# Optimization experiments

Measured on AMD Instinct MI355X. Metric: run time of the kernel, lower is better.

## Reference

```python
import jax, jax.numpy as jnp
import numpy as np

B, C, N, F = 256, 4, 64, 256   # batch, in_channels, neighbors, in_features
OC, OF = 8, 256                # out_channels, out_features


def setup_inputs() -> dict:
    key = jax.random.key(0)
    k1, k2, k3, k4, k5 = jax.random.split(key, 5)
    x = jax.random.normal(k1, (B, C, F), dtype=jnp.float32)
    neighbor = jax.random.normal(k2, (B, N, C, F), dtype=jnp.float32)
    # torch.nn.Linear weights are (out_features, in_features)
    W_att1 = jax.random.normal(k3, (C, F), dtype=jnp.float32) / np.sqrt(F).astype(np.float32)
    W_att2 = jax.random.normal(k4, (C, F), dtype=jnp.float32) / np.sqrt(F).astype(np.float32)
    # Conv1d weight: (out_c*out_f, 2C, F); kernel_size==F makes it a dense contraction
    W_conv = jax.random.normal(k5, (OC * OF, 2 * C, F), dtype=jnp.float32) / np.sqrt(2 * C * F).astype(np.float32)
    return {"x": x, "neighbor": neighbor, "W_att1": W_att1, "W_att2": W_att2, "W_conv": W_conv}


def reference(x, neighbor, W_att1, W_att2, W_conv):
    # --- attention weights: einsum 'ci,nkl->n' = sum(att1(x_i)) * sum_{k,l} att2(y_i)[n]
    s1 = jnp.sum(x @ W_att1.T, axis=(1, 2))              # (B,)
    s2 = jnp.sum(neighbor @ W_att2.T, axis=(2, 3))       # (B, N)
    w = jax.nn.softmax(s1[:, None] * s2, axis=1)         # softmax over neighbors (dim 0 per-sample)

    # --- feature adjacency: einsum 'ca,ncb,n->cab' vectorized over batch
    fadj = jnp.einsum('bcx,bncy,bn->bcxy', x, neighbor, w)   # (B, C, F, F)
    fadj = fadj + jnp.swapaxes(fadj, -1, -2)
    # sgnroot
    fadj = jnp.sign(fadj) * jnp.sqrt(jnp.clip(jnp.abs(fadj), 1e-8, None))
    # row normalize over dim -2, NaN -> 0
    adj = fadj / (jnp.abs(fadj).sum(axis=-2, keepdims=True) + 1e-7)
    adj = jnp.where(jnp.isnan(adj), jnp.float32(0.0), adj)

    # --- transform: cat([adj @ x, x], channel) then full-width conv1d (dense contraction)
    h = jnp.einsum('bcxy,bcy->bcx', adj, x)              # (B, C, F)
    z = jnp.concatenate([h, x], axis=1)                  # (B, 2C, F)
    out = jnp.einsum('bcf,ocf->bo', z, W_conv).reshape(B, OC, OF)
    return out, adj
```

## Files before the change

kernel.cpp:

```cpp
#include <hip/hip_runtime.h>
#include <hip/hip_bf16.h>
#include <math.h>


typedef __bf16 bf16x8 __attribute__((ext_vector_type(8)));
typedef __bf16 bf16x4 __attribute__((ext_vector_type(4)));
typedef float f32x4 __attribute__((ext_vector_type(4)));

#define NB 256
#define NC 4
#define NN 64
#define NF 256
#define NO 2048

__global__ __launch_bounds__(256) void k_pre(
    const float* __restrict__ x, const float* __restrict__ nb,
    const float* __restrict__ W1, const float* __restrict__ W2,
    float* __restrict__ s1, float* __restrict__ s2)
{
  __shared__ float w2s[256], w1s[256];
  int t = threadIdx.x;
  int w = t >> 6, l = t & 63;

  w2s[t] = W2[t] + W2[256 + t] + W2[512 + t] + W2[768 + t];
  w1s[t] = W1[t] + W1[256 + t] + W1[512 + t] + W1[768 + t];
  __syncthreads();

  int gw = blockIdx.x * 4 + w;
  float4 wv2 = *(const float4*)&w2s[l * 4];
  float4 wv1 = *(const float4*)&w1s[l * 4];
  for (int task = gw; task < 16640; task += 8192) {
    bool isS2 = task < 16384;
    const float4* src = isS2 ? ((const float4*)nb + (size_t)task * 256)
                             : ((const float4*)x + (size_t)(task - 16384) * 256);
    float4 wv = isS2 ? wv2 : wv1;
    float val = 0.f;
    #pragma unroll
    for (int k = 0; k < 4; ++k) {
      float4 v = src[l + 64 * k];
      val += v.x * wv.x + v.y * wv.y + v.z * wv.z + v.w * wv.w;
    }
    for (int off = 32; off > 0; off >>= 1) val += __shfl_down(val, off);
    if (l == 0) {
      if (isS2) s2[task] = val;
      else s1[task - 16384] = val;
    }
  }
}

__global__ __launch_bounds__(256) void k_adj(
    const float* __restrict__ x, const float* __restrict__ nb,
    const float* __restrict__ Wc,
    const float* __restrict__ s1, const float* __restrict__ s2,
    float* __restrict__ adj, __hip_bfloat16* __restrict__ zbf,
    __hip_bfloat16* __restrict__ Wcb)
{
  __shared__ float xs[256], ns[256], invs[256], wsh[64];
  __shared__ float part[4][256];
  int t = threadIdx.x;
  int w = t >> 6, l = t & 63;
  int blk = blockIdx.x;
  int b = blk >> 2, c = blk & 3;

  {
    const float4* Wc4 = (const float4*)Wc;
    bf16x4* Wcb4 = (bf16x4*)Wcb;
    #pragma unroll
    for (int q = 0; q < 4; ++q) {
      int idx = blk * 1024 + q * 256 + t;
      float4 v = Wc4[idx];
      bf16x4 o = { (__bf16)v.x, (__bf16)v.y, (__bf16)v.z, (__bf16)v.w };
      Wcb4[idx] = o;
    }
  }

  if (t < 64) {
    float v = s1[b] * s2[b * 64 + t];
    float m = v;
    for (int off = 32; off > 0; off >>= 1) m = fmaxf(m, __shfl_xor(m, off));
    float e = expf(v - m);
    float s = e;
    for (int off = 32; off > 0; off >>= 1) s += __shfl_xor(s, off);
    wsh[t] = e / s;
  }
  float xval = x[(size_t)blk * 256 + t];
  xs[t] = xval;
  zbf[(size_t)b * 2048 + 1024 + c * 256 + t] = __float2bfloat16(xval);
  __syncthreads();

  const float4* nb4 = (const float4*)(nb + (size_t)b * 65536 + c * 256);
  float4 a4 = {0.f, 0.f, 0.f, 0.f};
  #pragma unroll
  for (int k = 0; k < 16; ++k) {
    int n = w + 4 * k;
    float4 v = nb4[(size_t)n * 256 + l];
    float wn = wsh[n];
    a4.x = fmaf(wn, v.x, a4.x);
    a4.y = fmaf(wn, v.y, a4.y);
    a4.z = fmaf(wn, v.z, a4.z);
    a4.w = fmaf(wn, v.w, a4.w);
  }
  *(float4*)&part[w][l * 4] = a4;
  __syncthreads();
  ns[t] = part[0][t] + part[1][t] + part[2][t] + part[3][t];
  __syncthreads();

  int j0 = l * 4;
  float4 xv = *(const float4*)&xs[j0];
  float4 nv = *(const float4*)&ns[j0];
  int i0 = w * 64;

  float4 cs = {0.f, 0.f, 0.f, 0.f};
  #pragma unroll 4
  for (int ii = 0; ii < 64; ++ii) {
    int i = i0 + ii;
    float xi = xs[i], ni = ns[i];
    cs.x += __builtin_amdgcn_sqrtf(fmaxf(fabsf(fmaf(xi, nv.x, xv.x * ni)), 1e-8f));
    cs.y += __builtin_amdgcn_sqrtf(fmaxf(fabsf(fmaf(xi, nv.y, xv.y * ni)), 1e-8f));
    cs.z += __builtin_amdgcn_sqrtf(fmaxf(fabsf(fmaf(xi, nv.z, xv.z * ni)), 1e-8f));
    cs.w += __builtin_amdgcn_sqrtf(fmaxf(fabsf(fmaf(xi, nv.w, xv.w * ni)), 1e-8f));
  }
  *(float4*)&part[w][j0] = cs;
  __syncthreads();
  invs[t] = 1.f / (part[0][t] + part[1][t] + part[2][t] + part[3][t] + 1e-7f);
  __syncthreads();

  float4 iv = *(const float4*)&invs[j0];
  float4 ha = {0.f, 0.f, 0.f, 0.f};
  float* ab = adj + (size_t)blk * 65536;
  #pragma unroll 4
  for (int ii = 0; ii < 64; ++ii) {
    int i = i0 + ii;
    float xi = xs[i], ni = ns[i];
    float pix = invs[i] * xi;
    float v0 = fmaf(xi, nv.x, xv.x * ni);
    float v1 = fmaf(xi, nv.y, xv.y * ni);
    float v2 = fmaf(xi, nv.z, xv.z * ni);
    float v3 = fmaf(xi, nv.w, xv.w * ni);
    float g0 = copysignf(__builtin_amdgcn_sqrtf(fmaxf(fabsf(v0), 1e-8f)), v0);
    float g1 = copysignf(__builtin_amdgcn_sqrtf(fmaxf(fabsf(v1), 1e-8f)), v1);
    float g2 = copysignf(__builtin_amdgcn_sqrtf(fmaxf(fabsf(v2), 1e-8f)), v2);
    float g3 = copysignf(__builtin_amdgcn_sqrtf(fmaxf(fabsf(v3), 1e-8f)), v3);
    f32x4 o = { g0 * iv.x, g1 * iv.y, g2 * iv.z, g3 * iv.w };
    __builtin_nontemporal_store(o, (f32x4*)&ab[(size_t)i * 256 + j0]);
    ha.x = fmaf(g0, pix, ha.x);
    ha.y = fmaf(g1, pix, ha.y);
    ha.z = fmaf(g2, pix, ha.z);
    ha.w = fmaf(g3, pix, ha.w);
  }
  __syncthreads();
  *(float4*)&part[w][j0] = ha;
  __syncthreads();
  float hsum = part[0][t] + part[1][t] + part[2][t] + part[3][t];
  zbf[(size_t)b * 2048 + c * 256 + t] = __float2bfloat16(hsum);
}

__global__ __launch_bounds__(256) void k_gemm(
    const __hip_bfloat16* __restrict__ zb, const __hip_bfloat16* __restrict__ Wcb,
    float* __restrict__ out)
{
  __shared__ __hip_bfloat16 Al[2][64][136];
  __shared__ __hip_bfloat16 Bl[2][64][136];
  int t = threadIdx.x;
  int wave = t >> 6, lane = t & 63;
  int g = lane >> 4, r = lane & 15;
  int mh = wave >> 1, nh = wave & 1;
  int bm = blockIdx.x & 3, bn = blockIdx.x >> 2;

  f32x4 acc00 = {0.f,0.f,0.f,0.f}, acc01 = {0.f,0.f,0.f,0.f};
  f32x4 acc10 = {0.f,0.f,0.f,0.f}, acc11 = {0.f,0.f,0.f,0.f};

  const float4* zb4 = (const float4*)zb;
  const float4* wc4 = (const float4*)Wcb;

  #pragma unroll
  for (int q = 0; q < 4; ++q) {
    int idx = q * 256 + t;
    int row = idx >> 4, c16 = idx & 15;
    float4 va = zb4[(size_t)(bm * 64 + row) * 256 + c16];
    *(float4*)&Al[0][row][c16 * 8] = va;
    float4 vb = wc4[(size_t)(bn * 64 + row) * 256 + c16];
    *(float4*)&Bl[0][row][c16 * 8] = vb;
  }
  __syncthreads();

  int cur = 0;
  for (int kb = 0; kb < 16; ++kb) {
    float4 va[4], vb[4];
    if (kb < 15) {
      #pragma unroll
      for (int q = 0; q < 4; ++q) {
        int idx = q * 256 + t;
        int row = idx >> 4, c16 = idx & 15;
        va[q] = zb4[(size_t)(bm * 64 + row) * 256 + (kb + 1) * 16 + c16];
        vb[q] = wc4[(size_t)(bn * 64 + row) * 256 + (kb + 1) * 16 + c16];
      }
    }
    #pragma unroll
    for (int kk = 0; kk < 4; ++kk) {
      bf16x8 a0 = *(const bf16x8*)&Al[cur][mh * 32 + r][kk * 32 + g * 8];
      bf16x8 a1 = *(const bf16x8*)&Al[cur][mh * 32 + 16 + r][kk * 32 + g * 8];
      bf16x8 b0 = *(const bf16x8*)&Bl[cur][nh * 32 + r][kk * 32 + g * 8];
      bf16x8 b1 = *(const bf16x8*)&Bl[cur][nh * 32 + 16 + r][kk * 32 + g * 8];
      acc00 = __builtin_amdgcn_mfma_f32_16x16x32_bf16(a0, b0, acc00, 0, 0, 0);
      acc01 = __builtin_amdgcn_mfma_f32_16x16x32_bf16(a0, b1, acc01, 0, 0, 0);
      acc10 = __builtin_amdgcn_mfma_f32_16x16x32_bf16(a1, b0, acc10, 0, 0, 0);
      acc11 = __builtin_amdgcn_mfma_f32_16x16x32_bf16(a1, b1, acc11, 0, 0, 0);
    }
    if (kb < 15) {
      #pragma unroll
      for (int q = 0; q < 4; ++q) {
        int idx = q * 256 + t;
        int row = idx >> 4, c16 = idx & 15;
        *(float4*)&Al[cur ^ 1][row][c16 * 8] = va[q];
        *(float4*)&Bl[cur ^ 1][row][c16 * 8] = vb[q];
      }
    }
    __syncthreads();
    cur ^= 1;
  }

  int row0 = bm * 64 + mh * 32 + g * 4;
  int col0 = bn * 64 + nh * 32 + r;
  #pragma unroll
  for (int q = 0; q < 4; ++q) {
    __builtin_nontemporal_store(acc00[q], &out[(size_t)(row0 + q) * 2048 + col0]);
    __builtin_nontemporal_store(acc01[q], &out[(size_t)(row0 + q) * 2048 + col0 + 16]);
    __builtin_nontemporal_store(acc10[q], &out[(size_t)(row0 + 16 + q) * 2048 + col0]);
    __builtin_nontemporal_store(acc11[q], &out[(size_t)(row0 + 16 + q) * 2048 + col0 + 16]);
  }
}

__global__ __launch_bounds__(256) void k_scores_fb(
    const float* __restrict__ x, const float* __restrict__ nb,
    const float* __restrict__ W1, const float* __restrict__ W2,
    float* __restrict__ s1, float* __restrict__ s2)
{
  __shared__ float red[4];
  int t = threadIdx.x;
  int gid = blockIdx.x;
  float val;
  if (gid < NB * NN) {
    float w = W2[t] + W2[256 + t] + W2[512 + t] + W2[768 + t];
    const float* p = nb + (size_t)gid * 1024;
    val = w * (p[t] + p[256 + t] + p[512 + t] + p[768 + t]);
  } else {
    int b = gid - NB * NN;
    float w = W1[t] + W1[256 + t] + W1[512 + t] + W1[768 + t];
    const float* p = x + (size_t)b * 1024;
    val = w * (p[t] + p[256 + t] + p[512 + t] + p[768 + t]);
  }
  for (int off = 32; off > 0; off >>= 1) val += __shfl_down(val, off);
  if ((t & 63) == 0) red[t >> 6] = val;
  __syncthreads();
  if (t == 0) {
    float s = red[0] + red[1] + red[2] + red[3];
    if (gid < NB * NN) s2[gid] = s;
    else s1[gid - NB * NN] = s;
  }
}

__global__ __launch_bounds__(256) void k_adj_fb(
    const float* __restrict__ x, const float* __restrict__ nb,
    const float* __restrict__ s1, const float* __restrict__ s2,
    float* __restrict__ adj, float* __restrict__ hf)
{
  __shared__ float xs[256], ns[256], invs[256], wsh[64];
  __shared__ float part[4][256];
  int t = threadIdx.x;
  int w = t >> 6, l = t & 63;
  int blk = blockIdx.x;
  int b = blk >> 2, c = blk & 3;

  if (t < 64) {
    float v = s1[b] * s2[b * 64 + t];
    float m = v;
    for (int off = 32; off > 0; off >>= 1) m = fmaxf(m, __shfl_xor(m, off));
    float e = expf(v - m);
    float s = e;
    for (int off = 32; off > 0; off >>= 1) s += __shfl_xor(s, off);
    wsh[t] = e / s;
  }
  __syncthreads();
  float acc = 0.f;
  const float* pb = nb + (size_t)b * 65536 + c * 256 + t;
  #pragma unroll 8
  for (int n = 0; n < 64; ++n) acc = fmaf(wsh[n], pb[(size_t)n * 1024], acc);
  ns[t] = acc;
  xs[t] = x[(size_t)blk * 256 + t];
  __syncthreads();

  int j0 = l * 4;
  float4 xv = *(const float4*)&xs[j0];
  float4 nv = *(const float4*)&ns[j0];
  int i0 = w * 64;
  float4 cs = {0.f, 0.f, 0.f, 0.f};
  for (int ii = 0; ii < 64; ++ii) {
    int i = i0 + ii;
    float xi = xs[i], ni = ns[i];
    cs.x += __builtin_amdgcn_sqrtf(fmaxf(fabsf(fmaf(xi, nv.x, xv.x * ni)), 1e-8f));
    cs.y += __builtin_amdgcn_sqrtf(fmaxf(fabsf(fmaf(xi, nv.y, xv.y * ni)), 1e-8f));
    cs.z += __builtin_amdgcn_sqrtf(fmaxf(fabsf(fmaf(xi, nv.z, xv.z * ni)), 1e-8f));
    cs.w += __builtin_amdgcn_sqrtf(fmaxf(fabsf(fmaf(xi, nv.w, xv.w * ni)), 1e-8f));
  }
  *(float4*)&part[w][j0] = cs;
  __syncthreads();
  invs[t] = 1.f / (part[0][t] + part[1][t] + part[2][t] + part[3][t] + 1e-7f);
  __syncthreads();

  float4 iv = *(const float4*)&invs[j0];
  float4 ha = {0.f, 0.f, 0.f, 0.f};
  float* ab = adj + (size_t)blk * 65536;
  for (int ii = 0; ii < 64; ++ii) {
    int i = i0 + ii;
    float xi = xs[i], ni = ns[i];
    float pix = invs[i] * xi;
    float v0 = fmaf(xi, nv.x, xv.x * ni);
    float v1 = fmaf(xi, nv.y, xv.y * ni);
    float v2 = fmaf(xi, nv.z, xv.z * ni);
    float v3 = fmaf(xi, nv.w, xv.w * ni);
    float g0 = copysignf(__builtin_amdgcn_sqrtf(fmaxf(fabsf(v0), 1e-8f)), v0);
    float g1 = copysignf(__builtin_amdgcn_sqrtf(fmaxf(fabsf(v1), 1e-8f)), v1);
    float g2 = copysignf(__builtin_amdgcn_sqrtf(fmaxf(fabsf(v2), 1e-8f)), v2);
    float g3 = copysignf(__builtin_amdgcn_sqrtf(fmaxf(fabsf(v3), 1e-8f)), v3);
    f32x4 o = { g0 * iv.x, g1 * iv.y, g2 * iv.z, g3 * iv.w };
    *(f32x4*)&ab[(size_t)i * 256 + j0] = o;
    ha.x = fmaf(g0, pix, ha.x);
    ha.y = fmaf(g1, pix, ha.y);
    ha.z = fmaf(g2, pix, ha.z);
    ha.w = fmaf(g3, pix, ha.w);
  }
  __syncthreads();
  *(float4*)&part[w][j0] = ha;
  __syncthreads();
  hf[(size_t)blk * 256 + t] = part[0][t] + part[1][t] + part[2][t] + part[3][t];
}

__device__ inline bf16x8 cvt8_p(const float* p) {
  const float4* q = reinterpret_cast<const float4*>(p);
  float4 a = q[0], bq = q[1];
  bf16x8 r;
  r[0] = (__bf16)a.x;  r[1] = (__bf16)a.y;  r[2] = (__bf16)a.z;  r[3] = (__bf16)a.w;
  r[4] = (__bf16)bq.x; r[5] = (__bf16)bq.y; r[6] = (__bf16)bq.z; r[7] = (__bf16)bq.w;
  return r;
}

__global__ __launch_bounds__(256) void k_gemm_f32(
    const float* __restrict__ h, const float* __restrict__ x,
    const float* __restrict__ Wc, float* __restrict__ out)
{
  int tid = threadIdx.x;
  int wave = tid >> 6, lane = tid & 63;
  int g = lane >> 4, r = lane & 15;
  int bm = blockIdx.x & 3, bn = blockIdx.x >> 2;
  int m0 = bm * 64 + wave * 16;
  int n0 = bn * 32;
  int arow = m0 + r;
  int koff = g * 8;

  const float* za = h + (size_t)arow * 1024 + koff;
  const float* zb = x + (size_t)arow * 1024 + koff;
  const float* w0 = Wc + (size_t)(n0 + r) * 2048 + koff;
  const float* w1 = Wc + (size_t)(n0 + 16 + r) * 2048 + koff;

  f32x4 acc0 = {0.f, 0.f, 0.f, 0.f}, acc1 = {0.f, 0.f, 0.f, 0.f};
  #pragma unroll 4
  for (int ks = 0; ks < 32; ++ks) {
    acc0 = __builtin_amdgcn_mfma_f32_16x16x32_bf16(cvt8_p(za + ks * 32), cvt8_p(w0 + ks * 32), acc0, 0, 0, 0);
    acc1 = __builtin_amdgcn_mfma_f32_16x16x32_bf16(cvt8_p(za + ks * 32), cvt8_p(w1 + ks * 32), acc1, 0, 0, 0);
  }
  #pragma unroll 4
  for (int ks = 0; ks < 32; ++ks) {
    acc0 = __builtin_amdgcn_mfma_f32_16x16x32_bf16(cvt8_p(zb + ks * 32), cvt8_p(w0 + 1024 + ks * 32), acc0, 0, 0, 0);
    acc1 = __builtin_amdgcn_mfma_f32_16x16x32_bf16(cvt8_p(zb + ks * 32), cvt8_p(w1 + 1024 + ks * 32), acc1, 0, 0, 0);
  }
  #pragma unroll
  for (int q = 0; q < 4; ++q) {
    int row = m0 + g * 4 + q;
    out[(size_t)row * 2048 + n0 + r]      = acc0[q];
    out[(size_t)row * 2048 + n0 + 16 + r] = acc1[q];
  }
}

extern "C" void kernel_launch(void* const* d_in, const int* in_sizes, int n_in,
                              void* d_out, int out_size, void* d_ws, size_t ws_size,
                              hipStream_t stream) {
  const float* x  = (const float*)d_in[0];
  const float* nb = (const float*)d_in[1];
  const float* W1 = (const float*)d_in[2];
  const float* W2 = (const float*)d_in[3];
  const float* Wc = (const float*)d_in[4];
  float* out = (float*)d_out;
  float* adj = out + (size_t)NB * NO;

  char* ws = (char*)d_ws;
  const size_t ZBF_B = 1048576;
  const size_t WCB_B = 8388608;
  const size_t FREG = (256 + 16384) * 4;
  bool fast = ws_size >= ZBF_B + WCB_B + FREG;

  if (fast) {
    __hip_bfloat16* zbf = (__hip_bfloat16*)ws;
    __hip_bfloat16* Wcb = (__hip_bfloat16*)(ws + ZBF_B);
    float* s1  = (float*)(ws + ZBF_B + WCB_B);
    float* s2  = s1 + 256;
    k_pre<<<2048, 256, 0, stream>>>(x, nb, W1, W2, s1, s2);
    k_adj<<<NB * NC, 256, 0, stream>>>(x, nb, Wc, s1, s2, adj, zbf, Wcb);
    k_gemm<<<128, 256, 0, stream>>>(zbf, Wcb, out);
  } else {
    float* hws = (float*)d_ws;
    float* s1  = hws + 262144;
    float* s2  = s1 + 256;
    k_scores_fb<<<NB * NN + NB, 256, 0, stream>>>(x, nb, W1, W2, s1, s2);
    k_adj_fb<<<NB * NC, 256, 0, stream>>>(x, nb, s1, s2, adj, hws);
    k_gemm_f32<<<256, 256, 0, stream>>>(hws, x, Wc, out);
  }
}
```

Measured before the change: 95.20 us.

## Restructure adjacency kernel to one column per thread and two blocks per CTA

Each thread now owns one column j of the FxF adjacency tile and loops over all 256 rows itself, so column sums and the h reduction no longer need cross-wave partial buffers and several barriers. The softmax weights are kept in registers and broadcast with shuffles instead of shared memory. Each CTA handles two (b,c) slices with half as many blocks, and double-buffered shared arrays let the second iteration skip a barrier. Adj stores become scalar stores strided by row instead of float4 stores, and fewer blocks may reduce latency hiding.

```diff
diff --git a/kernel.cpp b/kernel.cpp
--- a/kernel.cpp
+++ b/kernel.cpp
@@ -55,104 +55,107 @@
     float* __restrict__ adj, __hip_bfloat16* __restrict__ zbf,
     __hip_bfloat16* __restrict__ Wcb)
 {
-  __shared__ float xs[256], ns[256], invs[256], wsh[64];
-  __shared__ float part[4][256];
+  __shared__ float xsb[2][256], nsb[2][256], pixb[2][256];
   int t = threadIdx.x;
-  int w = t >> 6, l = t & 63;
-  int blk = blockIdx.x;
-  int b = blk >> 2, c = blk & 3;
+  int l = t & 63;
+  int blk0 = blockIdx.x;
 
   {
     const float4* Wc4 = (const float4*)Wc;
     bf16x4* Wcb4 = (bf16x4*)Wcb;
     #pragma unroll
-    for (int q = 0; q < 4; ++q) {
-      int idx = blk * 1024 + q * 256 + t;
+    for (int q = 0; q < 8; ++q) {
+      int idx = blk0 * 2048 + q * 256 + t;
       float4 v = Wc4[idx];
       bf16x4 o = { (__bf16)v.x, (__bf16)v.y, (__bf16)v.z, (__bf16)v.w };
       Wcb4[idx] = o;
     }
   }
 
-  if (t < 64) {
-    float v = s1[b] * s2[b * 64 + t];
-    float m = v;
-    for (int off = 32; off > 0; off >>= 1) m = fmaxf(m, __shfl_xor(m, off));
-    float e = expf(v - m);
-    float s = e;
-    for (int off = 32; off > 0; off >>= 1) s += __shfl_xor(s, off);
-    wsh[t] = e / s;
-  }
-  float xval = x[(size_t)blk * 256 + t];
-  xs[t] = xval;
-  zbf[(size_t)b * 2048 + 1024 + c * 256 + t] = __float2bfloat16(xval);
-  __syncthreads();
-
-  const float4* nb4 = (const float4*)(nb + (size_t)b * 65536 + c * 256);
-  float4 a4 = {0.f, 0.f, 0.f, 0.f};
-  #pragma unroll
-  for (int k = 0; k < 16; ++k) {
-    int n = w + 4 * k;
-    float4 v = nb4[(size_t)n * 256 + l];
-    float wn = wsh[n];
-    a4.x = fmaf(wn, v.x, a4.x);
-    a4.y = fmaf(wn, v.y, a4.y);
-    a4.z = fmaf(wn, v.z, a4.z);
-    a4.w = fmaf(wn, v.w, a4.w);
-  }
-  *(float4*)&part[w][l * 4] = a4;
-  __syncthreads();
-  ns[t] = part[0][t] + part[1][t] + part[2][t] + part[3][t];
-  __syncthreads();
-
-  int j0 = l * 4;
-  float4 xv = *(const float4*)&xs[j0];
-  float4 nv = *(const float4*)&ns[j0];
-  int i0 = w * 64;
-
-  float4 cs = {0.f, 0.f, 0.f, 0.f};
-  #pragma unroll 4
-  for (int ii = 0; ii < 64; ++ii) {
-    int i = i0 + ii;
-    float xi = xs[i], ni = ns[i];
-    cs.x += __builtin_amdgcn_sqrtf(fmaxf(fabsf(fmaf(xi, nv.x, xv.x * ni)), 1e-8f));
-    cs.y += __builtin_amdgcn_sqrtf(fmaxf(fabsf(fmaf(xi, nv.y, xv.y * ni)), 1e-8f));
-    cs.z += __builtin_amdgcn_sqrtf(fmaxf(fabsf(fmaf(xi, nv.z, xv.z * ni)), 1e-8f));
-    cs.w += __builtin_amdgcn_sqrtf(fmaxf(fabsf(fmaf(xi, nv.w, xv.w * ni)), 1e-8f));
-  }
-  *(float4*)&part[w][j0] = cs;
-  __syncthreads();
-  invs[t] = 1.f / (part[0][t] + part[1][t] + part[2][t] + part[3][t] + 1e-7f);
-  __syncthreads();
-
-  float4 iv = *(const float4*)&invs[j0];
-  float4 ha = {0.f, 0.f, 0.f, 0.f};
-  float* ab = adj + (size_t)blk * 65536;
-  #pragma unroll 4
-  for (int ii = 0; ii < 64; ++ii) {
-    int i = i0 + ii;
-    float xi = xs[i], ni = ns[i];
-    float pix = invs[i] * xi;
-    float v0 = fmaf(xi, nv.x, xv.x * ni);
-    float v1 = fmaf(xi, nv.y, xv.y * ni);
-    float v2 = fmaf(xi, nv.z, xv.z * ni);
-    float v3 = fmaf(xi, nv.w, xv.w * ni);
-    float g0 = copysignf(__builtin_amdgcn_sqrtf(fmaxf(fabsf(v0), 1e-8f)), v0);
-    float g1 = copysignf(__builtin_amdgcn_sqrtf(fmaxf(fabsf(v1), 1e-8f)), v1);
-    float g2 = copysignf(__builtin_amdgcn_sqrtf(fmaxf(fabsf(v2), 1e-8f)), v2);
-    float g3 = copysignf(__builtin_amdgcn_sqrtf(fmaxf(fabsf(v3), 1e-8f)), v3);
-    f32x4 o = { g0 * iv.x, g1 * iv.y, g2 * iv.z, g3 * iv.w };
-    __builtin_nontemporal_store(o, (f32x4*)&ab[(size_t)i * 256 + j0]);
-    ha.x = fmaf(g0, pix, ha.x);
-    ha.y = fmaf(g1, pix, ha.y);
-    ha.z = fmaf(g2, pix, ha.z);
-    ha.w = fmaf(g3, pix, ha.w);
-  }
-  __syncthreads();
-  *(float4*)&part[w][j0] = ha;
-  __syncthreads();
-  float hsum = part[0][t] + part[1][t] + part[2][t] + part[3][t];
-  zbf[(size_t)b * 2048 + c * 256 + t] = __float2bfloat16(hsum);
+  for (int rep = 0; rep < 2; ++rep) {
+    int blk = blk0 + rep * 512;
+    int b = blk >> 2, c = blk & 3;
+    float* xs  = xsb[rep];
+    float* ns  = nsb[rep];
+    float* pix = pixb[rep];
+
+    float wsl;
+    {
+      float v = s1[b] * s2[b * 64 + l];
+      float m = v;
+      for (int off = 32; off > 0; off >>= 1) m = fmaxf(m, __shfl_xor(m, off));
+      float e = expf(v - m);
+      float s = e;
+      for (int off = 32; off > 0; off >>= 1) s += __shfl_xor(s, off);
+      wsl = e / s;
+    }
+
+    const float* nbp = nb + (size_t)b * 65536 + c * 256 + t;
+    float a0 = 0.f, a1 = 0.f, a2 = 0.f, a3 = 0.f;
+    #pragma unroll
+    for (int n = 0; n < 64; n += 4) {
+      float w0 = __shfl(wsl, n),     w1 = __shfl(wsl, n + 1);
+      float w2 = __shfl(wsl, n + 2), w3 = __shfl(wsl, n + 3);
+      a0 = fmaf(w0, nbp[(size_t)n * 1024],       a0);
+      a1 = fmaf(w1, nbp[(size_t)(n + 1) * 1024], a1);
+      a2 = fmaf(w2, nbp[(size_t)(n + 2) * 1024], a2);
+      a3 = fmaf(w3, nbp[(size_t)(n + 3) * 1024], a3);
+    }
+    float nst = (a0 + a1) + (a2 + a3);
+    float xt = x[(size_t)blk * 256 + t];
+    xs[t] = xt;
+    ns[t] = nst;
+    zbf[(size_t)b * 2048 + 1024 + c * 256 + t] = __float2bfloat16(xt);
+    asm volatile("s_waitcnt lgkmcnt(0)" ::: "memory");
+    __builtin_amdgcn_s_barrier();
+    asm volatile("" ::: "memory");
+
+    float cs0 = 0.f, cs1 = 0.f, cs2 = 0.f, cs3 = 0.f;
+    #pragma unroll 8
+    for (int i4 = 0; i4 < 64; ++i4) {
+      float4 x4 = *(const float4*)&xs[i4 * 4];
+      float4 n4 = *(const float4*)&ns[i4 * 4];
+      float v0 = fmaf(x4.x, nst, xt * n4.x);
+      float v1 = fmaf(x4.y, nst, xt * n4.y);
+      float v2 = fmaf(x4.z, nst, xt * n4.z);
+      float v3 = fmaf(x4.w, nst, xt * n4.w);
+      cs0 += __builtin_amdgcn_sqrtf(fmaxf(fabsf(v0), 1e-8f));
+      cs1 += __builtin_amdgcn_sqrtf(fmaxf(fabsf(v1), 1e-8f));
+      cs2 += __builtin_amdgcn_sqrtf(fmaxf(fabsf(v2), 1e-8f));
+      cs3 += __builtin_amdgcn_sqrtf(fmaxf(fabsf(v3), 1e-8f));
+    }
+    float invt = 1.f / (((cs0 + cs1) + (cs2 + cs3)) + 1e-7f);
+    pix[t] = invt * xt;
+    asm volatile("s_waitcnt lgkmcnt(0)" ::: "memory");
+    __builtin_amdgcn_s_barrier();
+    asm volatile("" ::: "memory");
+
+    float ha0 = 0.f, ha1 = 0.f;
+    float* ab = adj + (size_t)blk * 65536 + t;
+    #pragma unroll 4
+    for (int i4 = 0; i4 < 64; ++i4) {
+      float4 x4 = *(const float4*)&xs[i4 * 4];
+      float4 n4 = *(const float4*)&ns[i4 * 4];
+      float4 p4 = *(const float4*)&pix[i4 * 4];
+      float v0 = fmaf(x4.x, nst, xt * n4.x);
+      float v1 = fmaf(x4.y, nst, xt * n4.y);
+      float v2 = fmaf(x4.z, nst, xt * n4.z);
+      float v3 = fmaf(x4.w, nst, xt * n4.w);
+      float g0 = copysignf(__builtin_amdgcn_sqrtf(fmaxf(fabsf(v0), 1e-8f)), v0);
+      float g1 = copysignf(__builtin_amdgcn_sqrtf(fmaxf(fabsf(v1), 1e-8f)), v1);
+      float g2 = copysignf(__builtin_amdgcn_sqrtf(fmaxf(fabsf(v2), 1e-8f)), v2);
+      float g3 = copysignf(__builtin_amdgcn_sqrtf(fmaxf(fabsf(v3), 1e-8f)), v3);
+      __builtin_nontemporal_store(g0 * invt, ab + (size_t)(i4 * 4 + 0) * 256);
+      __builtin_nontemporal_store(g1 * invt, ab + (size_t)(i4 * 4 + 1) * 256);
+      __builtin_nontemporal_store(g2 * invt, ab + (size_t)(i4 * 4 + 2) * 256);
+      __builtin_nontemporal_store(g3 * invt, ab + (size_t)(i4 * 4 + 3) * 256);
+      ha0 = fmaf(g0, p4.x, ha0);
+      ha1 = fmaf(g1, p4.y, ha1);
+      ha0 = fmaf(g2, p4.z, ha0);
+      ha1 = fmaf(g3, p4.w, ha1);
+    }
+    zbf[(size_t)b * 2048 + c * 256 + t] = __float2bfloat16(ha0 + ha1);
+  }
 }
 
 __global__ __launch_bounds__(256) void k_gemm(
@@ -405,7 +408,7 @@
     float* s1  = (float*)(ws + ZBF_B + WCB_B);
     float* s2  = s1 + 256;
     k_pre<<<2048, 256, 0, stream>>>(x, nb, W1, W2, s1, s2);
-    k_adj<<<NB * NC, 256, 0, stream>>>(x, nb, Wc, s1, s2, adj, zbf, Wcb);
+    k_adj<<<512, 256, 0, stream>>>(x, nb, Wc, s1, s2, adj, zbf, Wcb);
     k_gemm<<<128, 256, 0, stream>>>(zbf, Wcb, out);
   } else {
     float* hws = (float*)d_ws;
```

Measured after the change: 96.13 us. About the same (+1.0%).

## Split conv GEMM: compute x-half in pre-kernel, h-half in final GEMM

Applied to the files above, without the earlier changes.

The x-dependent half of the final conv contraction (the K range over x channels) is computed early by 256 extra blocks in the pre-kernel, converting fp32 to bf16 on the fly and writing partial outputs. The final GEMM now loops over only the h half of K and adds the stored partial sums when writing results. This aims to take work off the critical path and overlap it with the memory-bound score pass, at the cost of an extra read and write of the output, on-the-fly conversion in the early blocks, and an assumption that k_adj writes zbf and Wcb in the layout the halved loop expects.

```diff
diff --git a/kernel.cpp b/kernel.cpp
--- a/kernel.cpp
+++ b/kernel.cpp
@@ -13,15 +13,53 @@
 #define NF 256
 #define NO 2048
 
+__device__ inline bf16x8 cvt8_p(const float* p) {
+  const float4* q = reinterpret_cast<const float4*>(p);
+  float4 a = q[0], bq = q[1];
+  bf16x8 r;
+  r[0] = (__bf16)a.x;  r[1] = (__bf16)a.y;  r[2] = (__bf16)a.z;  r[3] = (__bf16)a.w;
+  r[4] = (__bf16)bq.x; r[5] = (__bf16)bq.y; r[6] = (__bf16)bq.z; r[7] = (__bf16)bq.w;
+  return r;
+}
+
 __global__ __launch_bounds__(256) void k_pre(
     const float* __restrict__ x, const float* __restrict__ nb,
     const float* __restrict__ W1, const float* __restrict__ W2,
-    float* __restrict__ s1, float* __restrict__ s2)
+    const float* __restrict__ Wc,
+    float* __restrict__ s1, float* __restrict__ s2, float* __restrict__ outp)
 {
   __shared__ float w2s[256], w1s[256];
   int t = threadIdx.x;
+
+  if (blockIdx.x >= 2048) {
+    int id = blockIdx.x - 2048;
+    int wave = t >> 6, lane = t & 63;
+    int g = lane >> 4, r = lane & 15;
+    int bm = id & 3, bn = id >> 2;
+    int m0 = bm * 64 + wave * 16;
+    int n0 = bn * 32;
+    int arow = m0 + r;
+    int koff = g * 8;
+    const float* zx = x  + (size_t)arow * 1024 + koff;
+    const float* w0 = Wc + (size_t)(n0 + r) * 2048 + 1024 + koff;
+    const float* w1p = Wc + (size_t)(n0 + 16 + r) * 2048 + 1024 + koff;
+    f32x4 acc0 = {0.f,0.f,0.f,0.f}, acc1 = {0.f,0.f,0.f,0.f};
+    #pragma unroll 4
+    for (int ks = 0; ks < 32; ++ks) {
+      bf16x8 a = cvt8_p(zx + ks * 32);
+      acc0 = __builtin_amdgcn_mfma_f32_16x16x32_bf16(a, cvt8_p(w0 + ks * 32), acc0, 0, 0, 0);
+      acc1 = __builtin_amdgcn_mfma_f32_16x16x32_bf16(a, cvt8_p(w1p + ks * 32), acc1, 0, 0, 0);
+    }
+    #pragma unroll
+    for (int q = 0; q < 4; ++q) {
+      int row = m0 + g * 4 + q;
+      outp[(size_t)row * 2048 + n0 + r]      = acc0[q];
+      outp[(size_t)row * 2048 + n0 + 16 + r] = acc1[q];
+    }
+    return;
+  }
+
   int w = t >> 6, l = t & 63;
-
   w2s[t] = W2[t] + W2[256 + t] + W2[512 + t] + W2[768 + t];
   w1s[t] = W1[t] + W1[256 + t] + W1[512 + t] + W1[768 + t];
   __syncthreads();
@@ -185,9 +223,9 @@
   __syncthreads();
 
   int cur = 0;
-  for (int kb = 0; kb < 16; ++kb) {
+  for (int kb = 0; kb < 8; ++kb) {
     float4 va[4], vb[4];
-    if (kb < 15) {
+    if (kb < 7) {
       #pragma unroll
       for (int q = 0; q < 4; ++q) {
         int idx = q * 256 + t;
@@ -207,7 +245,7 @@
       acc10 = __builtin_amdgcn_mfma_f32_16x16x32_bf16(a1, b0, acc10, 0, 0, 0);
       acc11 = __builtin_amdgcn_mfma_f32_16x16x32_bf16(a1, b1, acc11, 0, 0, 0);
     }
-    if (kb < 15) {
+    if (kb < 7) {
       #pragma unroll
       for (int q = 0; q < 4; ++q) {
         int idx = q * 256 + t;
@@ -224,10 +262,14 @@
   int col0 = bn * 64 + nh * 32 + r;
   #pragma unroll
   for (int q = 0; q < 4; ++q) {
-    __builtin_nontemporal_store(acc00[q], &out[(size_t)(row0 + q) * 2048 + col0]);
-    __builtin_nontemporal_store(acc01[q], &out[(size_t)(row0 + q) * 2048 + col0 + 16]);
-    __builtin_nontemporal_store(acc10[q], &out[(size_t)(row0 + 16 + q) * 2048 + col0]);
-    __builtin_nontemporal_store(acc11[q], &out[(size_t)(row0 + 16 + q) * 2048 + col0 + 16]);
+    float p00 = out[(size_t)(row0 + q) * 2048 + col0];
+    float p01 = out[(size_t)(row0 + q) * 2048 + col0 + 16];
+    float p10 = out[(size_t)(row0 + 16 + q) * 2048 + col0];
+    float p11 = out[(size_t)(row0 + 16 + q) * 2048 + col0 + 16];
+    __builtin_nontemporal_store(acc00[q] + p00, &out[(size_t)(row0 + q) * 2048 + col0]);
+    __builtin_nontemporal_store(acc01[q] + p01, &out[(size_t)(row0 + q) * 2048 + col0 + 16]);
+    __builtin_nontemporal_store(acc10[q] + p10, &out[(size_t)(row0 + 16 + q) * 2048 + col0]);
+    __builtin_nontemporal_store(acc11[q] + p11, &out[(size_t)(row0 + 16 + q) * 2048 + col0 + 16]);
   }
 }
 
@@ -336,15 +378,6 @@
   hf[(size_t)blk * 256 + t] = part[0][t] + part[1][t] + part[2][t] + part[3][t];
 }
 
-__device__ inline bf16x8 cvt8_p(const float* p) {
-  const float4* q = reinterpret_cast<const float4*>(p);
-  float4 a = q[0], bq = q[1];
-  bf16x8 r;
-  r[0] = (__bf16)a.x;  r[1] = (__bf16)a.y;  r[2] = (__bf16)a.z;  r[3] = (__bf16)a.w;
-  r[4] = (__bf16)bq.x; r[5] = (__bf16)bq.y; r[6] = (__bf16)bq.z; r[7] = (__bf16)bq.w;
-  return r;
-}
-
 __global__ __launch_bounds__(256) void k_gemm_f32(
     const float* __restrict__ h, const float* __restrict__ x,
     const float* __restrict__ Wc, float* __restrict__ out)
@@ -404,7 +437,7 @@
     __hip_bfloat16* Wcb = (__hip_bfloat16*)(ws + ZBF_B);
     float* s1  = (float*)(ws + ZBF_B + WCB_B);
     float* s2  = s1 + 256;
-    k_pre<<<2048, 256, 0, stream>>>(x, nb, W1, W2, s1, s2);
+    k_pre<<<2304, 256, 0, stream>>>(x, nb, W1, W2, Wc, s1, s2, out);
     k_adj<<<NB * NC, 256, 0, stream>>>(x, nb, Wc, s1, s2, adj, zbf, Wcb);
     k_gemm<<<128, 256, 0, stream>>>(zbf, Wcb, out);
   } else {
```

New measurement: 155.6 us. 1.63x slower.
